# Performance work log

Hardware: AMD Instinct MI355X
Metric: run time of the kernel (lower is better)

The kernel has to match this reference:

```python
import jax, jax.numpy as jnp
import numpy as np

BN_EPS = 1e-5


def _bn(x, g, b, m, v):
    # inference-mode BatchNorm1d over channel dim of [B, C, N]
    return g[:, None] * (x - m[:, None]) * jax.lax.rsqrt(v[:, None] + BN_EPS) + b[:, None]


def _conv1x1(w, x):
    # Conv1d kernel_size=1, no bias: [O, C] x [B, C, N] -> [B, O, N]
    return jnp.einsum('oc,bcn->bon', w, x)


def setup_inputs() -> dict:
    key = jax.random.key(0)
    ks = jax.random.split(key, 32)
    B, N = 8, 4096

    def w(k, sh):
        return jax.random.normal(k, sh, jnp.float32) * 0.05

    def bn_params(k, c):
        k0, k1, k2, k3 = jax.random.split(k, 4)
        g = 1.0 + 0.1 * jax.random.normal(k0, (c,), jnp.float32)
        b = 0.1 * jax.random.normal(k1, (c,), jnp.float32)
        m = 0.1 * jax.random.normal(k2, (c,), jnp.float32)
        v = jax.random.uniform(k3, (c,), jnp.float32, 0.5, 1.5)
        return g, b, m, v

    g1, b1, m1, v1 = bn_params(ks[2], 64)
    gq, bq, mq, vq = bn_params(ks[3], 16)
    gk, bk, mk, vk = bn_params(ks[4], 16)
    gv, bv, mv, vv = bn_params(ks[5], 3)

    return {
        'x': jax.random.normal(ks[0], (B, 3, N), jnp.float32),
        'w1': w(ks[6], (64, 3)),
        'g1': g1, 'b1': b1, 'm1': m1, 'v1': v1,
        'w2': w(ks[7], (128, 64)),
        'wq': w(ks[8], (16, 128)),
        'gq': gq, 'bq': bq, 'mq': mq, 'vq': vq,
        'wk': w(ks[9], (16, 128)),
        'gk': gk, 'bk': bk, 'mk': mk, 'vk': vk,
        'wv': w(ks[10], (3, 128)),
        'gv': gv, 'bv': bv, 'mv': mv, 'vv': vv,
        'alpha': 0.1 * jax.random.normal(ks[11], (1,), jnp.float32),
        'offset': 0.1 * jax.random.normal(ks[12], (1,), jnp.float32),
    }


def reference(x, w1, g1, b1, m1, v1, w2,
              wq, gq, bq, mq, vq,
              wk, gk, bk, mk, vk,
              wv, gv, bv, mv, vv,
              alpha, offset):
    # mlp: conv(3->64) -> BN -> ReLU -> conv(64->128)
    feat = _conv1x1(w2, jax.nn.relu(_bn(_conv1x1(w1, x + offset), g1, b1, m1, v1)))  # [B,128,N]
    q = jax.nn.relu(_bn(_conv1x1(wq, feat), gq, bq, mq, vq))  # [B,16,N]
    k = jax.nn.relu(_bn(_conv1x1(wk, feat), gk, bk, mk, vk))  # [B,16,N]
    energy = jnp.einsum('bcn,bcm->bnm', q, k)                 # [B,N,N] (Q^T K)
    sim = jax.nn.softmax(energy, axis=-1)
    # offset-attention: column-wise L1 renormalization
    sim = sim / (1e-9 + sim.sum(axis=1, keepdims=True))
    v_ = jax.nn.relu(_bn(_conv1x1(wv, feat), gv, bv, mv, vv))  # [B,3,N]
    out = jnp.einsum('bcn,bnm->bcm', v_, sim)                  # [B,3,N]
    return alpha * out + x
```

## Files before the change

kernel.cpp:

```cpp
#include <hip/hip_runtime.h>

#define NPTS 4096
#define NB   8
#define BN_EPS 1e-5f
#define LOG2E 1.4426950408889634f
#define RS_SLICES 8
#define CS_SLICES 4

typedef float f32x16 __attribute__((ext_vector_type(16)));
typedef float f32x4  __attribute__((ext_vector_type(4)));
typedef short bf16x8 __attribute__((ext_vector_type(8)));
typedef unsigned short ushort_t;

#if __has_builtin(__builtin_amdgcn_exp2f)
#define EXP2(x) __builtin_amdgcn_exp2f(x)
#else
#define EXP2(x) exp2f(x)
#endif

__device__ __forceinline__ ushort_t f2bf(float f) {
    unsigned u = __builtin_bit_cast(unsigned, f);
    unsigned r = (u + 0x7FFFu + ((u >> 16) & 1u)) >> 16;
    return (ushort_t)r;
}

__global__ __launch_bounds__(256) void k0_prep(
    const float* __restrict__ w1, const float* __restrict__ g1, const float* __restrict__ b1,
    const float* __restrict__ m1, const float* __restrict__ v1,
    const float* __restrict__ w2,
    const float* __restrict__ wq, const float* __restrict__ gq, const float* __restrict__ bq,
    const float* __restrict__ mq, const float* __restrict__ vq,
    const float* __restrict__ wk, const float* __restrict__ gk, const float* __restrict__ bk,
    const float* __restrict__ mk, const float* __restrict__ vk,
    const float* __restrict__ wv, const float* __restrict__ gv, const float* __restrict__ bv,
    const float* __restrict__ mv, const float* __restrict__ vv,
    float* __restrict__ Wc, float* __restrict__ tb,
    float* __restrict__ w1s, float* __restrict__ t1)
{
    const int j = blockIdx.x;
    const int t = threadIdx.x;
    if (j == 35) {
        if (t < 64) {
            float s = g1[t] * rsqrtf(v1[t] + BN_EPS);
            w1s[t*3+0] = s * w1[t*3+0];
            w1s[t*3+1] = s * w1[t*3+1];
            w1s[t*3+2] = s * w1[t*3+2];
            t1[t] = b1[t] - s * m1[t];
        }
        return;
    }
    __shared__ float red[256];
    const int c = t & 63;
    const int chunk = t >> 6;
    const float* wrow;
    float g, bb, mm, vr, post = 1.f;
    if (j < 16)      { wrow = wq + j*128;      g = gq[j];    bb = bq[j];    mm = mq[j];    vr = vq[j];    post = LOG2E; }
    else if (j < 32) { int u = j-16; wrow = wk + u*128; g = gk[u]; bb = bk[u]; mm = mk[u]; vr = vk[u]; }
    else             { int u = j-32; wrow = wv + u*128; g = gv[u]; bb = bv[u]; mm = mv[u]; vr = vv[u]; }
    float acc = 0.f;
    for (int o = chunk*32; o < chunk*32 + 32; ++o) acc = fmaf(wrow[o], w2[o*64 + c], acc);
    red[t] = acc;
    __syncthreads();
    if (t < 64) {
        const float s4 = red[t] + red[64+t] + red[128+t] + red[192+t];
        const float sbn = g * rsqrtf(vr + BN_EPS);
        Wc[j*64 + t] = post * sbn * s4;
        if (t == 0) tb[j] = post * (bb - sbn * mm);
    }
}

__global__ __launch_bounds__(128) void k1_mlp(
    const float* __restrict__ x, const float* __restrict__ offset,
    const float* __restrict__ Wc, const float* __restrict__ tb,
    const float* __restrict__ w1s, const float* __restrict__ t1,
    ushort_t* __restrict__ qbuf, ushort_t* __restrict__ kbuf, float* __restrict__ aux)
{
    const int p = blockIdx.x*128 + threadIdx.x;
    const int b = p >> 12;
    const int n = p & 4095;
    const float off = offset[0];
    const float* xb = x + (size_t)b*3*NPTS + n;
    const float x0 = xb[0] + off, x1 = xb[NPTS] + off, x2 = xb[2*NPTS] + off;

    float acc[35];
#pragma unroll
    for (int j = 0; j < 35; ++j) acc[j] = tb[j];

    for (int c = 0; c < 64; ++c) {
        const float h = fmaxf(
            fmaf(w1s[c*3+0], x0, fmaf(w1s[c*3+1], x1, fmaf(w1s[c*3+2], x2, t1[c]))), 0.f);
        const float* wc = Wc + c;
#pragma unroll
        for (int j = 0; j < 35; ++j) acc[j] = fmaf(wc[j*64], h, acc[j]);
    }

    unsigned qw[8], kw[8];
#pragma unroll
    for (int i = 0; i < 8; ++i) {
        ushort_t qlo = f2bf(fmaxf(acc[2*i],    0.f));
        ushort_t qhi = f2bf(fmaxf(acc[2*i+1],  0.f));
        qw[i] = (unsigned)qlo | ((unsigned)qhi << 16);
        ushort_t klo = f2bf(fmaxf(acc[16+2*i],   0.f));
        ushort_t khi = f2bf(fmaxf(acc[16+2*i+1], 0.f));
        kw[i] = (unsigned)klo | ((unsigned)khi << 16);
    }
    uint4* qd = (uint4*)(qbuf + (size_t)p*16);
    qd[0] = make_uint4(qw[0], qw[1], qw[2], qw[3]);
    qd[1] = make_uint4(qw[4], qw[5], qw[6], qw[7]);
    uint4* kd = (uint4*)(kbuf + (size_t)p*16);
    kd[0] = make_uint4(kw[0], kw[1], kw[2], kw[3]);
    kd[1] = make_uint4(kw[4], kw[5], kw[6], kw[7]);
    float4* ar = (float4*)(aux + (size_t)p*4);
    *ar = make_float4(fmaxf(acc[32], 0.f), fmaxf(acc[33], 0.f), fmaxf(acc[34], 0.f), 0.f);
}

__global__ __launch_bounds__(256, 8) void k2_rowsum(
    const ushort_t* __restrict__ qbuf, const ushort_t* __restrict__ kbuf,
    float* __restrict__ psum)
{
    const int lane = threadIdx.x & 63;
    const int w = blockIdx.x*4 + (threadIdx.x >> 6);
    const int b = w >> 10;
    const int r = w & 1023;
    const int nblk = r >> 3;
    const int slice = r & 7;
    const int n0 = nblk * 32;
    const int m0 = slice * 512;

    const bf16x8 qfrag = *(const bf16x8*)(qbuf + ((size_t)b*NPTS + n0 + (lane & 31))*16 + (lane >> 5)*8);
    const ushort_t* kb = kbuf + ((size_t)b*NPTS + m0 + (lane & 31))*16 + (lane >> 5)*8;

    float rsum = 0.f;
    bf16x8 kf = *(const bf16x8*)kb;
    for (int t = 0; t < 16; ++t) {
        const bf16x8 kcur = kf;
        if (t + 1 < 16) kf = *(const bf16x8*)(kb + (size_t)(t+1)*512);
        f32x16 acc;
#pragma unroll
        for (int i = 0; i < 16; ++i) acc[i] = 0.f;
        acc = __builtin_amdgcn_mfma_f32_32x32x16_bf16(kcur, qfrag, acc, 0, 0, 0);
#pragma unroll
        for (int i = 0; i < 16; ++i) rsum += EXP2(acc[i]);
    }
    rsum += __shfl_xor(rsum, 32);
    if (lane < 32) psum[((size_t)slice*NB + b)*NPTS + n0 + lane] = rsum;
}

__global__ __launch_bounds__(256) void k3_rowred(
    const float* __restrict__ psum, float* __restrict__ aux)
{
    const int p = blockIdx.x*256 + threadIdx.x;
    const int b = p >> 12;
    const int n = p & 4095;
    float s = 0.f;
#pragma unroll
    for (int sl = 0; sl < RS_SLICES; ++sl) s += psum[((size_t)sl*NB + b)*NPTS + n];
    aux[(size_t)p*4 + 3] = 1.0f / s;
}

__global__ __launch_bounds__(256, 8) void k4_colpass(
    const ushort_t* __restrict__ qbuf, const ushort_t* __restrict__ kbuf,
    const float* __restrict__ aux, float* __restrict__ pcol)
{
    const int lane = threadIdx.x & 63;
    const int w = blockIdx.x*4 + (threadIdx.x >> 6);
    const int b = w >> 10;
    const int r = w & 1023;
    const int mtile = r >> 2;
    const int slice = r & 3;
    const int m0 = mtile * 16;
    const int n0 = slice * 1024;
    const int g = lane >> 4;
    const int lc = lane & 15;

    const bf16x8 zero8 = {0,0,0,0,0,0,0,0};
    bf16x8 afrag = zero8;
    if (g < 2) afrag = *(const bf16x8*)(kbuf + ((size_t)b*NPTS + m0 + lc)*16 + g*8);

    const ushort_t* qb = qbuf + ((size_t)b*NPTS + n0 + lc)*16 + g*8;
    const float4* auxp = (const float4*)aux + (size_t)b*NPTS + n0 + lc;

    float S[4]  = {0.f,0.f,0.f,0.f};
    float A0[4] = {0.f,0.f,0.f,0.f};
    float A1[4] = {0.f,0.f,0.f,0.f};
    float A2[4] = {0.f,0.f,0.f,0.f};

    bf16x8 qf = zero8;
    if (g < 2) qf = *(const bf16x8*)qb;
    float4 ax = auxp[0];
    for (int t = 0; t < 64; ++t) {
        const bf16x8 qcur = qf;
        const float4 axc = ax;
        if (t + 1 < 64) {
            if (g < 2) qf = *(const bf16x8*)(qb + (size_t)(t+1)*256);
            ax = auxp[(size_t)(t+1)*16];
        }
        f32x4 acc;
#pragma unroll
        for (int i = 0; i < 4; ++i) acc[i] = 0.f;
        acc = __builtin_amdgcn_mfma_f32_16x16x32_bf16(afrag, qcur, acc, 0, 0, 0);
#pragma unroll
        for (int i = 0; i < 4; ++i) {
            const float wgt = EXP2(acc[i]) * axc.w;
            S[i]  += wgt;
            A0[i] = fmaf(axc.x, wgt, A0[i]);
            A1[i] = fmaf(axc.y, wgt, A1[i]);
            A2[i] = fmaf(axc.z, wgt, A2[i]);
        }
    }

#pragma unroll
    for (int d = 1; d <= 8; d <<= 1) {
#pragma unroll
        for (int i = 0; i < 4; ++i) {
            S[i]  += __shfl_xor(S[i],  d);
            A0[i] += __shfl_xor(A0[i], d);
            A1[i] += __shfl_xor(A1[i], d);
            A2[i] += __shfl_xor(A2[i], d);
        }
    }

    if (lc == 0) {
        float* base = pcol + (((size_t)b*CS_SLICES + slice)*4)*NPTS;
#pragma unroll
        for (int i = 0; i < 4; ++i) {
            const int m = m0 + g*4 + i;
            base[0*NPTS + m] = S[i];
            base[1*NPTS + m] = A0[i];
            base[2*NPTS + m] = A1[i];
            base[3*NPTS + m] = A2[i];
        }
    }
}

__global__ __launch_bounds__(256) void k5_final(
    const float* __restrict__ pcol, const float* __restrict__ x,
    const float* __restrict__ alpha, float* __restrict__ out)
{
    const int p = blockIdx.x*256 + threadIdx.x;
    const int b = p >> 12;
    const int m = p & 4095;
    float s = 0.f, a0 = 0.f, a1 = 0.f, a2 = 0.f;
#pragma unroll
    for (int sl = 0; sl < CS_SLICES; ++sl) {
        const float* base = pcol + (((size_t)b*CS_SLICES + sl)*4)*NPTS;
        s  += base[0*NPTS + m];
        a0 += base[1*NPTS + m];
        a1 += base[2*NPTS + m];
        a2 += base[3*NPTS + m];
    }
    const float sc = alpha[0] / (1e-9f + s);
    const float* xb = x + (size_t)b*3*NPTS + m;
    float* ob = out + (size_t)b*3*NPTS + m;
    ob[0*NPTS] = fmaf(a0, sc, xb[0*NPTS]);
    ob[1*NPTS] = fmaf(a1, sc, xb[1*NPTS]);
    ob[2*NPTS] = fmaf(a2, sc, xb[2*NPTS]);
}

extern "C" void kernel_launch(void* const* d_in, const int* in_sizes, int n_in,
                              void* d_out, int out_size, void* d_ws, size_t ws_size,
                              hipStream_t stream) {
    const float* x      = (const float*)d_in[0];
    const float* w1     = (const float*)d_in[1];
    const float* g1     = (const float*)d_in[2];
    const float* b1     = (const float*)d_in[3];
    const float* m1     = (const float*)d_in[4];
    const float* v1     = (const float*)d_in[5];
    const float* w2     = (const float*)d_in[6];
    const float* wq     = (const float*)d_in[7];
    const float* gq     = (const float*)d_in[8];
    const float* bq     = (const float*)d_in[9];
    const float* mq     = (const float*)d_in[10];
    const float* vq     = (const float*)d_in[11];
    const float* wk     = (const float*)d_in[12];
    const float* gk     = (const float*)d_in[13];
    const float* bk     = (const float*)d_in[14];
    const float* mk     = (const float*)d_in[15];
    const float* vk     = (const float*)d_in[16];
    const float* wv     = (const float*)d_in[17];
    const float* gv     = (const float*)d_in[18];
    const float* bv     = (const float*)d_in[19];
    const float* mv     = (const float*)d_in[20];
    const float* vv     = (const float*)d_in[21];
    const float* alpha  = (const float*)d_in[22];
    const float* offset = (const float*)d_in[23];

    char* ws = (char*)d_ws;
    float*    Wc   = (float*)(ws + 0);
    float*    tb   = (float*)(ws + 16*1024);
    float*    w1s  = (float*)(ws + 32*1024);
    float*    t1   = (float*)(ws + 48*1024);
    ushort_t* qbuf = (ushort_t*)(ws + 64*1024);
    ushort_t* kbuf = (ushort_t*)(ws + 64*1024 + (size_t)1*1024*1024);
    float*    aux  = (float*)(ws + 64*1024 + (size_t)2*1024*1024);
    float*    psum = (float*)(ws + 64*1024 + (size_t)2*1024*1024 + 512*1024);
    float*    pcol = (float*)(ws + 64*1024 + (size_t)4*1024*1024);

    k0_prep<<<dim3(36), dim3(256), 0, stream>>>(
        w1, g1, b1, m1, v1, w2,
        wq, gq, bq, mq, vq,
        wk, gk, bk, mk, vk,
        wv, gv, bv, mv, vv,
        Wc, tb, w1s, t1);

    k1_mlp<<<dim3(256), dim3(128), 0, stream>>>(
        x, offset, Wc, tb, w1s, t1, qbuf, kbuf, aux);

    k2_rowsum<<<dim3(2048), dim3(256), 0, stream>>>(qbuf, kbuf, psum);
    k3_rowred<<<dim3(128), dim3(256), 0, stream>>>(psum, aux);
    k4_colpass<<<dim3(2048), dim3(256), 0, stream>>>(qbuf, kbuf, aux, pcol);
    k5_final<<<dim3(128), dim3(256), 0, stream>>>(pcol, x, alpha, (float*)d_out);
}
```

Baseline: 174.6 us.

## Switch column pass to 32x32 MFMA tiles and prescale values by row inverse

The column pass now uses the 32x32x16 bf16 MFMA over 32-column tiles instead of a 16x16x32 MFMA that left half the lanes zero-padded. This halves the wave count and removes wasted matrix work, at the cost of 64 accumulator registers per lane and lower occupancy (launch bound lowered to 4). The row-reduction kernel now folds the reciprocal row sum into the stored V values, which saves one multiply per element in the inner loop. The row-sum kernel gains two-deep prefetch and four independent accumulators to shorten dependency chains.

```diff
diff --git a/kernel.cpp b/kernel.cpp
--- a/kernel.cpp
+++ b/kernel.cpp
@@ -8,7 +8,6 @@
 #define CS_SLICES 4
 
 typedef float f32x16 __attribute__((ext_vector_type(16)));
-typedef float f32x4  __attribute__((ext_vector_type(4)));
 typedef short bf16x8 __attribute__((ext_vector_type(8)));
 typedef unsigned short ushort_t;
 
@@ -130,18 +129,27 @@
     const bf16x8 qfrag = *(const bf16x8*)(qbuf + ((size_t)b*NPTS + n0 + (lane & 31))*16 + (lane >> 5)*8);
     const ushort_t* kb = kbuf + ((size_t)b*NPTS + m0 + (lane & 31))*16 + (lane >> 5)*8;
 
-    float rsum = 0.f;
-    bf16x8 kf = *(const bf16x8*)kb;
+    float rs0 = 0.f, rs1 = 0.f, rs2 = 0.f, rs3 = 0.f;
+    bf16x8 kf0 = *(const bf16x8*)kb;
+    bf16x8 kf1 = *(const bf16x8*)(kb + 512);
     for (int t = 0; t < 16; ++t) {
-        const bf16x8 kcur = kf;
-        if (t + 1 < 16) kf = *(const bf16x8*)(kb + (size_t)(t+1)*512);
+        const bf16x8 kcur = kf0;
+        kf0 = kf1;
+        const int tn = (t + 2 < 16) ? t + 2 : 15;
+        kf1 = *(const bf16x8*)(kb + (size_t)tn*512);
         f32x16 acc;
 #pragma unroll
         for (int i = 0; i < 16; ++i) acc[i] = 0.f;
         acc = __builtin_amdgcn_mfma_f32_32x32x16_bf16(kcur, qfrag, acc, 0, 0, 0);
 #pragma unroll
-        for (int i = 0; i < 16; ++i) rsum += EXP2(acc[i]);
-    }
+        for (int i = 0; i < 16; i += 4) {
+            rs0 += EXP2(acc[i+0]);
+            rs1 += EXP2(acc[i+1]);
+            rs2 += EXP2(acc[i+2]);
+            rs3 += EXP2(acc[i+3]);
+        }
+    }
+    float rsum = (rs0 + rs1) + (rs2 + rs3);
     rsum += __shfl_xor(rsum, 32);
     if (lane < 32) psum[((size_t)slice*NB + b)*NPTS + n0 + lane] = rsum;
 }
@@ -155,64 +163,62 @@
     float s = 0.f;
 #pragma unroll
     for (int sl = 0; sl < RS_SLICES; ++sl) s += psum[((size_t)sl*NB + b)*NPTS + n];
-    aux[(size_t)p*4 + 3] = 1.0f / s;
-}
-
-__global__ __launch_bounds__(256, 8) void k4_colpass(
+    const float inv = 1.0f / s;
+    float4* ar = (float4*)(aux + (size_t)p*4);
+    float4 v = *ar;
+    *ar = make_float4(v.x*inv, v.y*inv, v.z*inv, inv);
+}
+
+__global__ __launch_bounds__(256, 4) void k4_colpass(
     const ushort_t* __restrict__ qbuf, const ushort_t* __restrict__ kbuf,
     const float* __restrict__ aux, float* __restrict__ pcol)
 {
     const int lane = threadIdx.x & 63;
     const int w = blockIdx.x*4 + (threadIdx.x >> 6);
-    const int b = w >> 10;
-    const int r = w & 1023;
+    const int b = w >> 9;
+    const int r = w & 511;
     const int mtile = r >> 2;
     const int slice = r & 3;
-    const int m0 = mtile * 16;
+    const int m0 = mtile * 32;
     const int n0 = slice * 1024;
-    const int g = lane >> 4;
-    const int lc = lane & 15;
-
-    const bf16x8 zero8 = {0,0,0,0,0,0,0,0};
-    bf16x8 afrag = zero8;
-    if (g < 2) afrag = *(const bf16x8*)(kbuf + ((size_t)b*NPTS + m0 + lc)*16 + g*8);
-
-    const ushort_t* qb = qbuf + ((size_t)b*NPTS + n0 + lc)*16 + g*8;
-    const float4* auxp = (const float4*)aux + (size_t)b*NPTS + n0 + lc;
-
-    float S[4]  = {0.f,0.f,0.f,0.f};
-    float A0[4] = {0.f,0.f,0.f,0.f};
-    float A1[4] = {0.f,0.f,0.f,0.f};
-    float A2[4] = {0.f,0.f,0.f,0.f};
-
-    bf16x8 qf = zero8;
-    if (g < 2) qf = *(const bf16x8*)qb;
-    float4 ax = auxp[0];
-    for (int t = 0; t < 64; ++t) {
-        const bf16x8 qcur = qf;
-        const float4 axc = ax;
-        if (t + 1 < 64) {
-            if (g < 2) qf = *(const bf16x8*)(qb + (size_t)(t+1)*256);
-            ax = auxp[(size_t)(t+1)*16];
-        }
-        f32x4 acc;
-#pragma unroll
-        for (int i = 0; i < 4; ++i) acc[i] = 0.f;
-        acc = __builtin_amdgcn_mfma_f32_16x16x32_bf16(afrag, qcur, acc, 0, 0, 0);
-#pragma unroll
-        for (int i = 0; i < 4; ++i) {
-            const float wgt = EXP2(acc[i]) * axc.w;
-            S[i]  += wgt;
-            A0[i] = fmaf(axc.x, wgt, A0[i]);
-            A1[i] = fmaf(axc.y, wgt, A1[i]);
-            A2[i] = fmaf(axc.z, wgt, A2[i]);
-        }
-    }
-
-#pragma unroll
-    for (int d = 1; d <= 8; d <<= 1) {
-#pragma unroll
-        for (int i = 0; i < 4; ++i) {
+
+    const bf16x8 afrag = *(const bf16x8*)(kbuf + ((size_t)b*NPTS + m0 + (lane & 31))*16 + (lane >> 5)*8);
+    const ushort_t* qb = qbuf + ((size_t)b*NPTS + n0 + (lane & 31))*16 + (lane >> 5)*8;
+    const float4* auxp = (const float4*)aux + (size_t)b*NPTS + n0 + (lane & 31);
+
+    float S[16], A0[16], A1[16], A2[16];
+#pragma unroll
+    for (int i = 0; i < 16; ++i) { S[i] = 0.f; A0[i] = 0.f; A1[i] = 0.f; A2[i] = 0.f; }
+
+    bf16x8 qf0 = *(const bf16x8*)qb;
+    bf16x8 qf1 = *(const bf16x8*)(qb + 512);
+    float4 ax0 = auxp[0];
+    float4 ax1 = auxp[32];
+    for (int t = 0; t < 32; ++t) {
+        const bf16x8 qcur = qf0;
+        const float4 axc = ax0;
+        qf0 = qf1; ax0 = ax1;
+        const int tn = (t + 2 < 32) ? t + 2 : 31;
+        qf1 = *(const bf16x8*)(qb + (size_t)tn*512);
+        ax1 = auxp[(size_t)tn*32];
+        f32x16 acc;
+#pragma unroll
+        for (int i = 0; i < 16; ++i) acc[i] = 0.f;
+        acc = __builtin_amdgcn_mfma_f32_32x32x16_bf16(afrag, qcur, acc, 0, 0, 0);
+#pragma unroll
+        for (int i = 0; i < 16; ++i) {
+            const float e1 = EXP2(acc[i]);
+            S[i]  = fmaf(axc.w, e1, S[i]);
+            A0[i] = fmaf(axc.x, e1, A0[i]);
+            A1[i] = fmaf(axc.y, e1, A1[i]);
+            A2[i] = fmaf(axc.z, e1, A2[i]);
+        }
+    }
+
+#pragma unroll
+    for (int d = 1; d <= 16; d <<= 1) {
+#pragma unroll
+        for (int i = 0; i < 16; ++i) {
             S[i]  += __shfl_xor(S[i],  d);
             A0[i] += __shfl_xor(A0[i], d);
             A1[i] += __shfl_xor(A1[i], d);
@@ -220,11 +226,12 @@
         }
     }
 
-    if (lc == 0) {
+    if ((lane & 31) == 0) {
+        const int hi = lane >> 5;
         float* base = pcol + (((size_t)b*CS_SLICES + slice)*4)*NPTS;
 #pragma unroll
-        for (int i = 0; i < 4; ++i) {
-            const int m = m0 + g*4 + i;
+        for (int i = 0; i < 16; ++i) {
+            const int m = m0 + (i & 3) + 8*(i >> 2) + 4*hi;
             base[0*NPTS + m] = S[i];
             base[1*NPTS + m] = A0[i];
             base[2*NPTS + m] = A1[i];
@@ -308,6 +315,6 @@
 
     k2_rowsum<<<dim3(2048), dim3(256), 0, stream>>>(qbuf, kbuf, psum);
     k3_rowred<<<dim3(128), dim3(256), 0, stream>>>(psum, aux);
-    k4_colpass<<<dim3(2048), dim3(256), 0, stream>>>(qbuf, kbuf, aux, pcol);
+    k4_colpass<<<dim3(1024), dim3(256), 0, stream>>>(qbuf, kbuf, aux, pcol);
     k5_final<<<dim3(128), dim3(256), 0, stream>>>(pcol, x, alpha, (float*)d_out);
 }
```

Result: faster. 165.6 us (-5.2%).
